# Performance work log

Hardware: AMD Instinct MI355X
Metric: run time of the kernel (lower is better)

The kernel has to match this reference:

```python
import jax, jax.numpy as jnp
import numpy as np

L = 24; CAP = 2 ** 18; F = 2; POS_DIM = 3; NR_ITERS_C2F = 10000
SCALES = np.geomspace(1.0, 1e-4, L).astype(np.float32)
PRIMES = np.array([1, 2654435761, 805459861], dtype=np.uint32)


def _sh4(d):
    # real spherical harmonics up to degree 4 (l=0..3) -> 16 features
    x, y, z = d[:, 0], d[:, 1], d[:, 2]
    xx, yy, zz = x * x, y * y, z * z
    return jnp.stack([
        jnp.full_like(x, 0.28209479177387814),
        -0.48860251190291987 * y, 0.48860251190291987 * z, -0.48860251190291987 * x,
        1.0925484305920792 * x * y, -1.0925484305920792 * y * z,
        0.94617469575755997 * zz - 0.31539156525251999,
        -1.0925484305920792 * x * z, 0.54627421529603959 * (xx - yy),
        -0.59004358992664352 * y * (3.0 * xx - yy),
        2.8906114426405538 * x * y * z,
        -0.45704579946446572 * y * (4.0 * zz - xx - yy),
        0.37317633259011546 * z * (2.0 * zz - 3.0 * xx - 3.0 * yy),
        -0.45704579946446572 * x * (4.0 * zz - xx - yy),
        1.4453057213202769 * z * (xx - yy),
        -0.59004358992664352 * x * (xx - 3.0 * yy),
    ], axis=1)


def _window(iter_nr):
    # map_range_val(iter,0,C,0.3,1.0) then cosine coarse-to-fine window per level
    t = 0.3 + 0.7 * min(max(float(iter_nr) / NR_ITERS_C2F, 0.0), 1.0)
    return 0.5 * (1.0 - jnp.cos(jnp.pi * jnp.clip(t * L - jnp.arange(L, dtype=jnp.float32), 0.0, 1.0)))


def _encode(pos, tables, shifts, window):
    # multi-res hash encoding: per-level gather of 8 cell corners + linear interp
    scales = jnp.asarray(SCALES)
    coords = pos[None, :, :] / scales[:, None, None]          # [L,N,3]
    fl = jnp.floor(coords)
    frac = coords - fl                                        # [L,N,3]
    base = fl.astype(jnp.int32) + shifts[:, None, :].astype(jnp.int32)
    primes = jnp.asarray(PRIMES)
    out = jnp.zeros((L, pos.shape[0], F), dtype=tables.dtype)
    for corner in range(8):  # fixed small loop over cell corners
        offs = jnp.array([(corner >> k) & 1 for k in range(3)], dtype=jnp.int32)
        c = (base + offs).astype(jnp.uint32)
        h = c * primes
        idx = (h[..., 0] ^ h[..., 1] ^ h[..., 2]) & jnp.uint32(CAP - 1)  # [L,N]
        w = jnp.prod(jnp.where(offs == 1, frac, 1.0 - frac), axis=-1)    # [L,N]
        feat = jax.vmap(lambda t, i: t[i])(tables, idx.astype(jnp.int32))  # [L,N,F] gather
        out = out + w[..., None] * feat
    out = out * window[:, None, None]
    feats = jnp.transpose(out, (1, 0, 2)).reshape(pos.shape[0], L * F)
    return jnp.concatenate([feats, pos], axis=1)  # concat_points, scaling=1 -> [N, 51]


def _lin_init(key, fan_in, fan_out):
    kw, kb = jax.random.split(key)
    w = jax.random.normal(kw, (fan_in, fan_out), dtype=jnp.float32) * np.sqrt(2.0 / fan_in)
    b = jnp.zeros((fan_out,), dtype=jnp.float32)
    return w, b


def setup_inputs() -> dict:
    key = jax.random.key(0)
    ks = jax.random.split(key, 12)
    N = 1 << 20
    samples_pos = jax.random.uniform(ks[0], (N, 3), minval=-1.0, maxval=1.0)
    d = jax.random.normal(ks[1], (N, 3), dtype=jnp.float32)
    samples_dirs = d / jnp.linalg.norm(d, axis=-1, keepdims=True)
    tables = jax.random.uniform(ks[2], (L, CAP, F), minval=-1e-4, maxval=1e-4)
    shifts = jax.random.randint(ks[3], (L, 3), 0, 100000, dtype=jnp.int32)
    W1, b1 = _lin_init(ks[4], 51, 64)
    W2, b2 = _lin_init(ks[5], 64, 64)
    W3, b3 = _lin_init(ks[6], 64, 64)
    W4, b4 = _lin_init(ks[7], 64, 65)
    R1, rb1 = _lin_init(ks[8], 80, 64)
    R2, rb2 = _lin_init(ks[9], 64, 64)
    R3, rb3 = _lin_init(ks[10], 64, 3)
    return dict(samples_pos=samples_pos, samples_dirs=samples_dirs, iter_nr=10000,
                tables=tables, shifts=shifts,
                W1=W1, b1=b1, W2=W2, b2=b2, W3=W3, b3=b3, W4=W4, b4=b4,
                R1=R1, rb1=rb1, R2=R2, rb2=rb2, R3=R3, rb3=rb3)


def reference(samples_pos, samples_dirs, iter_nr, tables, shifts,
              W1, b1, W2, b2, W3, b3, W4, b4, R1, rb1, R2, rb2, R3, rb3):
    window = _window(iter_nr)
    pf = _encode(samples_pos, tables, shifts, window)           # [N,51]
    sh = _sh4(samples_dirs)                                     # [N,16] (no grad in original)
    g = lambda x: jax.nn.gelu(x, approximate=False)             # torch GELU default = exact
    h = g(pf @ W1 + b1)
    h = g(h @ W2 + b2)
    h = g(h @ W3 + b3)
    fd = h @ W4 + b4                                            # [N,65]
    density = jax.nn.softplus(fd[:, 0:1])
    feat_rgb = fd[:, 1:65]
    hr = jnp.concatenate([g(feat_rgb), sh], axis=1)             # [N,80]
    hr = g(hr @ R1 + rb1)
    hr = g(hr @ R2 + rb2)
    rgb = jax.nn.sigmoid(hr @ R3 + rb3)                         # [N,3]
    return rgb, density
```

## Files before the change

kernel.cpp:

```cpp
#include <hip/hip_runtime.h>
#include <math.h>

typedef unsigned short u16;
typedef unsigned int   u32;

#define LVLS 24
#define CAPN (1 << 18)
#define STR  84
#define WAVES 8
#define TPW  16
#define ACTSZ (TPW * STR + 16)

#define WB1   0
#define WB2   4096
#define WB3   8192
#define WB4   12288
#define WBR1  16384
#define WBR2  22528
#define SWOFF 26624
#define W4C   26672
#define R3C   26736
#define SHF   26928
#define ACT0  27008
#define LDS_U32 (ACT0 + WAVES * ACTSZ)

typedef float    f32x4 __attribute__((ext_vector_type(4)));
typedef _Float16 f16x8 __attribute__((ext_vector_type(8)));
typedef u32      u32x4 __attribute__((ext_vector_type(4)));

#if __has_builtin(__builtin_amdgcn_rcpf)
#define RCPF(x) __builtin_amdgcn_rcpf(x)
#else
#define RCPF(x) (1.0f / (x))
#endif
#if __has_builtin(__builtin_amdgcn_exp2f)
#define EXP2F(x) __builtin_amdgcn_exp2f(x)
#else
#define EXP2F(x) exp2f(x)
#endif


__device__ __forceinline__ float h2f(u16 b) {
    union { u16 u; _Float16 h; } v; v.u = b; return (float)v.h;
}
__device__ __forceinline__ u16 f2h(float x) {
    union { _Float16 h; u16 u; } v; v.h = (_Float16)x; return v.u;
}
__device__ __forceinline__ void hsplit(float x, u16& h, u16& l) {
    h = f2h(x);
    float r = x - h2f(h);
    l = f2h(r);
}
__device__ __forceinline__ u32 packhl(float x) {
    u16 h, l; hsplit(x, h, l);
    return ((u32)h << 16) | l;
}
__device__ __forceinline__ float unpackhl(u32 w) {
    return h2f((u16)(w >> 16)) + h2f((u16)(w & 0xffffu));
}
__device__ __forceinline__ float gelu_f(float x) {
    float z  = fabsf(x) * 0.70710678118654752f;
    float t  = RCPF(fmaf(0.3275911f, z, 1.0f));
    float e  = EXP2F(-z * z * 1.44269504088896340f);
    float p  = fmaf(1.061405429f, t, -1.453152027f);
    p = fmaf(p, t, 1.421413741f);
    p = fmaf(p, t, -0.284496736f);
    p = fmaf(p, t, 0.254829592f);
    p = p * t;
    float erfv = fmaf(-p, e, 1.0f);
    float se   = copysignf(erfv, x);
    return x * fmaf(0.5f, se, 0.5f);
}
__device__ __forceinline__ float sigmoid_f(float y) {
    return RCPF(1.0f + EXP2F(-y * 1.44269504088896340f));
}
__device__ __forceinline__ f16x8 cast8h(u32 a, u32 b, u32 c, u32 d) {
    union { u32 u[4]; f16x8 h; } v; v.u[0]=a; v.u[1]=b; v.u[2]=c; v.u[3]=d; return v.h;
}
__device__ __forceinline__ f16x8 cast8hv(u32x4 u) {
    union { u32x4 u4; f16x8 h; } v; v.u4 = u; return v.h;
}
__device__ __forceinline__ void window_scale(int l, const int* iter, float& sc, float& wl) {
    sc = powf(10.0f, (float)l * (-4.0f / 23.0f));
    double itd = (double)iter[0] / 10000.0;
    itd = itd < 0.0 ? 0.0 : (itd > 1.0 ? 1.0 : itd);
    float tL = (float)((0.3 + 0.7 * itd) * 24.0);
    float arg = fminf(fmaxf(tL - (float)l, 0.0f), 1.0f);
    wl = 0.5f - 0.5f * cosf(3.14159265358979323846f * arg);
}

__device__ __forceinline__ void hash_level(float px, float py, float pz, float sc, float wl,
                                           int sx, int sy, int sz,
                                           const float* __restrict__ tl,
                                           float& f0, float& f1) {
    float cx = px / sc, cy = py / sc, cz = pz / sc;
    float fx = floorf(cx), fy = floorf(cy), fz = floorf(cz);
    float rx = cx - fx, ry = cy - fy, rz = cz - fz;
    int bx = (int)fx + sx, by = (int)fy + sy, bz = (int)fz + sz;
    u32 hx0 = (u32)bx, hx1 = (u32)(bx + 1);
    u32 hy0 = (u32)by * 2654435761u, hy1 = (u32)(by + 1) * 2654435761u;
    u32 hz0 = (u32)bz * 805459861u,  hz1 = (u32)(bz + 1) * 805459861u;
    float a0 = 0.f, a1 = 0.f;
    #pragma unroll
    for (int c = 0; c < 8; c++) {
        u32 hx = (c & 1) ? hx1 : hx0;
        u32 hy = (c & 2) ? hy1 : hy0;
        u32 hz = (c & 4) ? hz1 : hz0;
        u32 idx = (hx ^ hy ^ hz) & (CAPN - 1);
        float w = ((c & 1) ? rx : 1.0f - rx);
        w *= ((c & 2) ? ry : 1.0f - ry);
        w *= ((c & 4) ? rz : 1.0f - rz);
        float2 tf = *(const float2*)(tl + 2 * (size_t)idx);
        a0 = fmaf(w, tf.x, a0);
        a1 = fmaf(w, tf.y, a1);
    }
    f0 = a0 * wl;
    f1 = a1 * wl;
}

__device__ __forceinline__ void hash_level_part(float px, float py, float pz, float sc,
                                                int sx, int sy, int sz, int c0,
                                                const float* __restrict__ tl,
                                                float2& g0, float2& g1, float& w0, float& w1) {
    float cx = px / sc, cy = py / sc, cz = pz / sc;
    float fx = floorf(cx), fy = floorf(cy), fz = floorf(cz);
    float rx = cx - fx, ry = cy - fy, rz = cz - fz;
    int bx = (int)fx + sx, by = (int)fy + sy, bz = (int)fz + sz;
    #pragma unroll
    for (int cc = 0; cc < 2; cc++) {
        int c = c0 + cc;
        u32 hx = (u32)(bx + (c & 1));
        u32 hy = (u32)(by + ((c >> 1) & 1)) * 2654435761u;
        u32 hz = (u32)(bz + ((c >> 2) & 1)) * 805459861u;
        u32 idx = (hx ^ hy ^ hz) & (CAPN - 1);
        float w = ((c & 1) ? rx : 1.0f - rx)
                * ((c & 2) ? ry : 1.0f - ry)
                * ((c & 4) ? rz : 1.0f - rz);
        float2 tf = *(const float2*)(tl + 2 * (size_t)idx);
        if (cc == 0) { g0 = tf; w0 = w; } else { g1 = tf; w1 = w; }
    }
}

__device__ __forceinline__ void wavesync() {
    asm volatile("s_waitcnt lgkmcnt(0)" ::: "memory");
    __builtin_amdgcn_sched_barrier(0);
}

template <int NKT, bool SHT>
__device__ __forceinline__ void mfma_layer_lds(const u32* blob, const u32* actw,
                                               int lane, f32x4 acc[4]) {
    const int q = lane >> 4, r = lane & 15;
    const int half = NKT * 1024;
    #pragma unroll
    for (int it = 0; it < 4; it++) acc[it] = (f32x4){0.f, 0.f, 0.f, 0.f};
    #pragma unroll
    for (int kt = 0; kt < NKT; kt++) {
        f16x8 whi[4], wlo[4];
        #pragma unroll
        for (int it = 0; it < 4; it++) {
            const u32* pb = blob + ((it * NKT + kt) * 64 + lane) * 4;
            whi[it] = cast8hv(*(const u32x4*)pb);
            wlo[it] = cast8hv(*(const u32x4*)(pb + half));
        }
        bool zero = SHT && (kt == NKT - 1) && (q >= 2);
        const u32* rowp = actw + r * STR + kt * 32 + q * 8;
        u32x4 v0 = *(const u32x4*)rowp;
        u32x4 v1 = *(const u32x4*)(rowp + 4);
        if (zero) { v0 = (u32x4){0,0,0,0}; v1 = (u32x4){0,0,0,0}; }
        u32 v[8] = { v0.x, v0.y, v0.z, v0.w, v1.x, v1.y, v1.z, v1.w };
        u32 xh[4], xl[4];
        #pragma unroll
        for (int j2 = 0; j2 < 4; j2++) {
            xh[j2] = (v[2*j2] >> 16) | (v[2*j2+1] & 0xffff0000u);
            xl[j2] = (v[2*j2] & 0xffffu) | (v[2*j2+1] << 16);
        }
        f16x8 bh = cast8h(xh[0], xh[1], xh[2], xh[3]);
        f16x8 bl = cast8h(xl[0], xl[1], xl[2], xl[3]);
        #pragma unroll
        for (int it = 0; it < 4; it++) {
            acc[it] = __builtin_amdgcn_mfma_f32_16x16x32_f16(whi[it], bh, acc[it], 0, 0, 0);
            acc[it] = __builtin_amdgcn_mfma_f32_16x16x32_f16(whi[it], bl, acc[it], 0, 0, 0);
            acc[it] = __builtin_amdgcn_mfma_f32_16x16x32_f16(wlo[it], bh, acc[it], 0, 0, 0);
        }
    }
}

__device__ __forceinline__ void epilogue_gelu(f32x4 acc[4], const float* __restrict__ bias,
                                              u32* actw, int lane) {
    const int q = lane >> 4, r = lane & 15;
    #pragma unroll
    for (int it = 0; it < 4; it++) {
        int mb = it * 16 + q * 4;
        float c0 = bias[mb], c1 = bias[mb + 1], c2 = bias[mb + 2], c3 = bias[mb + 3];
        f32x4 d = acc[it];
        u32x4 wv;
        wv.x = packhl(gelu_f(fmaf(d[0], 0x1p-16f, c0)) * 256.0f);
        wv.y = packhl(gelu_f(fmaf(d[1], 0x1p-16f, c1)) * 256.0f);
        wv.z = packhl(gelu_f(fmaf(d[2], 0x1p-16f, c2)) * 256.0f);
        wv.w = packhl(gelu_f(fmaf(d[3], 0x1p-16f, c3)) * 256.0f);
        *(u32x4*)(actw + r * STR + mb) = wv;
    }
}

template <bool SPLIT>
__global__ void __launch_bounds__(512, 1) nerf_persist(
    const float* __restrict__ pos, const float* __restrict__ dirs,
    const int* __restrict__ iter, const float* __restrict__ tables,
    const int* __restrict__ shifts,
    const float* __restrict__ W1, const float* __restrict__ b1,
    const float* __restrict__ W2, const float* __restrict__ b2,
    const float* __restrict__ W3, const float* __restrict__ b3,
    const float* __restrict__ W4, const float* __restrict__ b4,
    const float* __restrict__ R1, const float* __restrict__ rb1,
    const float* __restrict__ R2, const float* __restrict__ rb2,
    const float* __restrict__ R3, const float* __restrict__ rb3,
    u32* __restrict__ pf,
    float* __restrict__ out, int n, int nbat, int ppb)
{
    extern __shared__ u32 lds[];
    const int tid  = threadIdx.x;
    const int lane = tid & 63;
    const int wave = tid >> 6;
    const int r = lane & 15;
    const int h = lane >> 4;

    {
        const float* Wp[6] = { W1, W2, W3, W4, R1, R2 };
        for (int e2 = tid; e2 < 13312; e2 += 512) {
            int p = e2, base, nkt, Ksrc, ldm, coloff, layer;
            if      (p < 2048)  { layer=0; base=WB1;  nkt=2; Ksrc=51; ldm=64; coloff=0; }
            else if (p < 4096)  { layer=1; base=WB2;  nkt=2; Ksrc=64; ldm=64; coloff=0; p-=2048; }
            else if (p < 6144)  { layer=2; base=WB3;  nkt=2; Ksrc=64; ldm=64; coloff=0; p-=4096; }
            else if (p < 8192)  { layer=3; base=WB4;  nkt=2; Ksrc=64; ldm=65; coloff=1; p-=6144; }
            else if (p < 11264) { layer=4; base=WBR1; nkt=3; Ksrc=80; ldm=64; coloff=0; p-=8192; }
            else                { layer=5; base=WBR2; nkt=2; Ksrc=64; ldm=64; coloff=0; p-=11264; }
            const float* W = Wp[layer];
            int j = p & 3, ln = (p >> 2) & 63, fk = p >> 8;
            int qq = ln >> 4, rr = ln & 15;
            int kt = fk % nkt, it = fk / nkt;
            int m  = it * 16 + rr;
            int k0 = kt * 32 + qq * 8 + 2 * j;
            float w0 = (k0     < Ksrc) ? W[(size_t)k0 * ldm + m + coloff] * 256.0f : 0.0f;
            float w1 = (k0 + 1 < Ksrc) ? W[(size_t)(k0 + 1) * ldm + m + coloff] * 256.0f : 0.0f;
            u16 h0, l0, h1, l1; hsplit(w0, h0, l0); hsplit(w1, h1, l1);
            int half = nkt * 1024;
            int idx  = base + (fk * 64 + ln) * 4 + j;
            lds[idx]        = (u32)h0 | ((u32)h1 << 16);
            lds[idx + half] = (u32)l0 | ((u32)l1 << 16);
        }
        if (tid < 24) {
            float sc, wl; window_scale(tid, iter, sc, wl);
            lds[SWOFF + 2*tid]     = __float_as_uint(sc);
            lds[SWOFF + 2*tid + 1] = __float_as_uint(wl);
        }
        if (tid >= 64 && tid < 128)  lds[W4C + tid - 64]  = __float_as_uint(W4[(size_t)(tid - 64) * 65]);
        if (tid >= 128 && tid < 320) lds[R3C + tid - 128] = __float_as_uint(R3[tid - 128]);
        if (tid >= 320 && tid < 392) lds[SHF + tid - 320] = (u32)shifts[tid - 320];
    }
    __syncthreads();

    u32* actw  = lds + ACT0 + wave * ACTSZ;
    u32* myrow = actw + r * STR;

    const int pbase = SPLIT ? blockIdx.x * ppb : 0;

    if constexpr (SPLIT) {
        for (int cp = 0; cp < ppb; cp += 512 * 8) {
            float lx[8], ly[8], lz[8];
            bool  lv[8];
            #pragma unroll
            for (int j = 0; j < 8; j++) {
                int off = cp + j * 512 + tid;
                int p = pbase + off;
                lv[j] = (off < ppb) && (p < n);
                lx[j] = 0.f; ly[j] = 0.f; lz[j] = 0.f;
                if (lv[j]) { lx[j] = pos[3*p]; ly[j] = pos[3*p+1]; lz[j] = pos[3*p+2]; }
            }
            for (int l = 0; l < LVLS; l++) {
                float sc = __uint_as_float(lds[SWOFF + 2*l]);
                float wl = __uint_as_float(lds[SWOFF + 2*l + 1]);
                int sx = (int)lds[SHF + 3*l], sy = (int)lds[SHF + 3*l + 1], sz = (int)lds[SHF + 3*l + 2];
                const float* tl = tables + 2 * ((size_t)l * CAPN);
                #pragma unroll 2
                for (int j = 0; j < 8; j++) {
                    if (!lv[j]) continue;
                    float f0, f1;
                    hash_level(lx[j], ly[j], lz[j], sc, wl, sx, sy, sz, tl, f0, f1);
                    int p = pbase + cp + j * 512 + tid;
                    pf[(size_t)l * n + p] = (u32)f2h(f0 * 256.0f) | ((u32)f2h(f1 * 256.0f) << 16);
                }
                __syncthreads();
            }
        }
        __syncthreads();
    }

    const int iters = SPLIT ? (ppb / (WAVES * TPW)) : nbat;
    for (int bb0 = 0; bb0 < iters; bb0++) {
        int tstart;
        if constexpr (SPLIT) {
            tstart = pbase + (bb0 * WAVES + wave) * TPW;
        } else {
            int bb = blockIdx.x + bb0 * gridDim.x;
            if (bb >= nbat) break;
            tstart = (bb * WAVES + wave) * TPW;
        }
        const bool tok = (tstart < n);
        const int i    = tstart + r;
        const bool valid = tok && (i < n);

        float px = 0.f, py = 0.f, pz = 0.f;
        if (valid) { px = pos[3*i]; py = pos[3*i+1]; pz = pos[3*i+2]; }

        if (tok && h == 0) {
            #pragma unroll
            for (int k = 51; k < 64; k++) myrow[k] = 0u;
            myrow[48] = packhl(px * 256.0f);
            myrow[49] = packhl(py * 256.0f);
            myrow[50] = packhl(pz * 256.0f);
        }

        if constexpr (SPLIT) {
            if (tok) {
                #pragma unroll
                for (int li = 0; li < 6; li++) {
                    int l = h * 6 + li;
                    u32 v = valid ? pf[(size_t)l * n + i] : 0u;
                    myrow[2*l]     = v << 16;
                    myrow[2*l + 1] = v & 0xffff0000u;
                }
            }
        } else {
            if (tok) {
                const int c0 = h * 2;
                #pragma unroll 2
                for (int l = 0; l < LVLS; l++) {
                    float sc = __uint_as_float(lds[SWOFF + 2*l]);
                    float wl = __uint_as_float(lds[SWOFF + 2*l + 1]);
                    int sx = (int)lds[SHF + 3*l], sy = (int)lds[SHF + 3*l + 1], sz = (int)lds[SHF + 3*l + 2];
                    float2 g0, g1; float w0, w1;
                    hash_level_part(px, py, pz, sc, sx, sy, sz, c0,
                                    tables + 2 * ((size_t)l * CAPN), g0, g1, w0, w1);
                    float a0 = fmaf(w0, g0.x, w1 * g1.x);
                    float a1 = fmaf(w0, g0.y, w1 * g1.y);
                    a0 += __shfl_xor(a0, 16); a0 += __shfl_xor(a0, 32);
                    a1 += __shfl_xor(a1, 16); a1 += __shfl_xor(a1, 32);
                    if (h == 0) {
                        myrow[2*l]     = (u32)f2h(a0 * wl * 256.0f) << 16;
                        myrow[2*l + 1] = (u32)f2h(a1 * wl * 256.0f) << 16;
                    }
                }
            }
        }
        wavesync();

        f32x4 acc[4];
        if (tok) { mfma_layer_lds<2, false>(lds + WB1, actw, lane, acc); epilogue_gelu(acc, b1, actw, lane); }
        wavesync();
        if (tok) { mfma_layer_lds<2, false>(lds + WB2, actw, lane, acc); epilogue_gelu(acc, b2, actw, lane); }
        wavesync();
        if (tok) { mfma_layer_lds<2, false>(lds + WB3, actw, lane, acc); epilogue_gelu(acc, b3, actw, lane); }
        wavesync();

        if (tok) {
            float t = 0.f;
            #pragma unroll
            for (int kk = 0; kk < 16; kk++) {
                int k = h * 16 + kk;
                t = fmaf(unpackhl(myrow[k]), __uint_as_float(lds[W4C + k]), t);
            }
            t += __shfl_xor(t, 16);
            t += __shfl_xor(t, 32);
            float s = fmaf(t, 0x1p-8f, b4[0]);
            if (h == 0 && valid) out[(size_t)3 * n + i] = fmaxf(s, 0.f) + log1pf(expf(-fabsf(s)));

            mfma_layer_lds<2, false>(lds + WB4, actw, lane, acc);
            epilogue_gelu(acc, b4 + 1, actw, lane);

            float dx = 0.f, dy = 0.f, dz = 0.f;
            if (valid) { dx = dirs[3*i]; dy = dirs[3*i+1]; dz = dirs[3*i+2]; }
            float xx = dx*dx, yy = dy*dy, zz = dz*dz;
            float sh[16];
            sh[0]  = 0.28209479177387814f;
            sh[1]  = -0.48860251190291987f * dy;
            sh[2]  = 0.48860251190291987f * dz;
            sh[3]  = -0.48860251190291987f * dx;
            sh[4]  = 1.0925484305920792f * dx * dy;
            sh[5]  = -1.0925484305920792f * dy * dz;
            sh[6]  = 0.94617469575756f * zz - 0.31539156525252f;
            sh[7]  = -1.0925484305920792f * dx * dz;
            sh[8]  = 0.5462742152960396f * (xx - yy);
            sh[9]  = -0.5900435899266435f * dy * (3.0f * xx - yy);
            sh[10] = 2.890611442640554f * dx * dy * dz;
            sh[11] = -0.4570457994644657f * dy * (4.0f * zz - xx - yy);
            sh[12] = 0.37317633259011546f * dz * (2.0f * zz - 3.0f * xx - 3.0f * yy);
            sh[13] = -0.4570457994644657f * dx * (4.0f * zz - xx - yy);
            sh[14] = 1.445305721320277f * dz * (xx - yy);
            sh[15] = -0.5900435899266435f * dx * (xx - 3.0f * yy);
            #pragma unroll
            for (int j = 0; j < 4; j++) myrow[64 + h * 4 + j] = packhl(sh[h * 4 + j] * 256.0f);
        }
        wavesync();

        if (tok) { mfma_layer_lds<3, true >(lds + WBR1, actw, lane, acc); epilogue_gelu(acc, rb1, actw, lane); }
        wavesync();
        if (tok) { mfma_layer_lds<2, false>(lds + WBR2, actw, lane, acc); epilogue_gelu(acc, rb2, actw, lane); }
        wavesync();

        if (tok) {
            float t0 = 0.f, t1 = 0.f, t2 = 0.f;
            #pragma unroll
            for (int kk = 0; kk < 16; kk++) {
                int k = h * 16 + kk;
                float xv = unpackhl(myrow[k]);
                t0 = fmaf(xv, __uint_as_float(lds[R3C + 3*k + 0]), t0);
                t1 = fmaf(xv, __uint_as_float(lds[R3C + 3*k + 1]), t1);
                t2 = fmaf(xv, __uint_as_float(lds[R3C + 3*k + 2]), t2);
            }
            t0 += __shfl_xor(t0, 16); t0 += __shfl_xor(t0, 32);
            t1 += __shfl_xor(t1, 16); t1 += __shfl_xor(t1, 32);
            t2 += __shfl_xor(t2, 16); t2 += __shfl_xor(t2, 32);
            if (h == 0 && valid) {
                float y0 = fmaf(t0, 0x1p-8f, rb3[0]);
                float y1 = fmaf(t1, 0x1p-8f, rb3[1]);
                float y2 = fmaf(t2, 0x1p-8f, rb3[2]);
                out[(size_t)3 * i + 0] = sigmoid_f(y0);
                out[(size_t)3 * i + 1] = sigmoid_f(y1);
                out[(size_t)3 * i + 2] = sigmoid_f(y2);
            }
        }
        wavesync();
    }
}

extern "C" void kernel_launch(void* const* d_in, const int* in_sizes, int n_in,
                              void* d_out, int out_size, void* d_ws, size_t ws_size,
                              hipStream_t stream) {
    int n = in_sizes[0] / 3;
    int ntiles = (n + TPW - 1) / TPW;
    int nbat = (ntiles + WAVES - 1) / WAVES;
    size_t ldsb = (size_t)LDS_U32 * 4;

    size_t need = (size_t)LVLS * (size_t)n * 4;
    bool split = (ws_size >= need) && (n >= 256 * WAVES * TPW);

    if (split) {
        int cpb = (n + 255) / 256;
        int ppb = (cpb + WAVES * TPW - 1) & ~(WAVES * TPW - 1);
        hipFuncSetAttribute(reinterpret_cast<const void*>(nerf_persist<true>),
                            hipFuncAttributeMaxDynamicSharedMemorySize, (int)ldsb);
        nerf_persist<true><<<256, 512, ldsb, stream>>>(
            (const float*)d_in[0], (const float*)d_in[1], (const int*)d_in[2],
            (const float*)d_in[3], (const int*)d_in[4],
            (const float*)d_in[5],  (const float*)d_in[6],
            (const float*)d_in[7],  (const float*)d_in[8],
            (const float*)d_in[9],  (const float*)d_in[10],
            (const float*)d_in[11], (const float*)d_in[12],
            (const float*)d_in[13], (const float*)d_in[14],
            (const float*)d_in[15], (const float*)d_in[16],
            (const float*)d_in[17], (const float*)d_in[18],
            (u32*)d_ws, (float*)d_out, n, nbat, ppb);
    } else {
        int grid = nbat < 256 ? nbat : 256;
        hipFuncSetAttribute(reinterpret_cast<const void*>(nerf_persist<false>),
                            hipFuncAttributeMaxDynamicSharedMemorySize, (int)ldsb);
        nerf_persist<false><<<grid, 512, ldsb, stream>>>(
            (const float*)d_in[0], (const float*)d_in[1], (const int*)d_in[2],
            (const float*)d_in[3], (const int*)d_in[4],
            (const float*)d_in[5],  (const float*)d_in[6],
            (const float*)d_in[7],  (const float*)d_in[8],
            (const float*)d_in[9],  (const float*)d_in[10],
            (const float*)d_in[11], (const float*)d_in[12],
            (const float*)d_in[13], (const float*)d_in[14],
            (const float*)d_in[15], (const float*)d_in[16],
            (const float*)d_in[17], (const float*)d_in[18],
            (u32*)d_ws, (float*)d_out, n, nbat, 0);
    }
}
```

Before: 1.044 ms.

## Keep MLP activations in registers and exchange via shuffles instead of LDS

Removes the per-wave LDS activation staging between MLP layers. Each layer's epilogue output now stays in registers, and the MFMA B operands are rebuilt with cross-lane shuffles, which also drops the wave-level LDS waits. LDS shrinks to the weights only, so the block grows to 16 waves (1024 threads) and the non-split hash path is restructured so each lane handles whole levels. The cost is more shuffle instructions and much higher register pressure per thread under the 1024-thread launch bound.

```diff
diff --git a/kernel.cpp b/kernel.cpp
--- a/kernel.cpp
+++ b/kernel.cpp
@@ -6,10 +6,8 @@
 
 #define LVLS 24
 #define CAPN (1 << 18)
-#define STR  84
-#define WAVES 8
+#define WAVES 16
 #define TPW  16
-#define ACTSZ (TPW * STR + 16)
 
 #define WB1   0
 #define WB2   4096
@@ -21,8 +19,7 @@
 #define W4C   26672
 #define R3C   26736
 #define SHF   26928
-#define ACT0  27008
-#define LDS_U32 (ACT0 + WAVES * ACTSZ)
+#define LDS_U32 27008
 
 typedef float    f32x4 __attribute__((ext_vector_type(4)));
 typedef _Float16 f16x8 __attribute__((ext_vector_type(8)));
@@ -118,39 +115,14 @@
     f1 = a1 * wl;
 }
 
-__device__ __forceinline__ void hash_level_part(float px, float py, float pz, float sc,
-                                                int sx, int sy, int sz, int c0,
-                                                const float* __restrict__ tl,
-                                                float2& g0, float2& g1, float& w0, float& w1) {
-    float cx = px / sc, cy = py / sc, cz = pz / sc;
-    float fx = floorf(cx), fy = floorf(cy), fz = floorf(cz);
-    float rx = cx - fx, ry = cy - fy, rz = cz - fz;
-    int bx = (int)fx + sx, by = (int)fy + sy, bz = (int)fz + sz;
-    #pragma unroll
-    for (int cc = 0; cc < 2; cc++) {
-        int c = c0 + cc;
-        u32 hx = (u32)(bx + (c & 1));
-        u32 hy = (u32)(by + ((c >> 1) & 1)) * 2654435761u;
-        u32 hz = (u32)(bz + ((c >> 2) & 1)) * 805459861u;
-        u32 idx = (hx ^ hy ^ hz) & (CAPN - 1);
-        float w = ((c & 1) ? rx : 1.0f - rx)
-                * ((c & 2) ? ry : 1.0f - ry)
-                * ((c & 4) ? rz : 1.0f - rz);
-        float2 tf = *(const float2*)(tl + 2 * (size_t)idx);
-        if (cc == 0) { g0 = tf; w0 = w; } else { g1 = tf; w1 = w; }
-    }
-}
-
-__device__ __forceinline__ void wavesync() {
-    asm volatile("s_waitcnt lgkmcnt(0)" ::: "memory");
-    __builtin_amdgcn_sched_barrier(0);
-}
-
-template <int NKT, bool SHT>
-__device__ __forceinline__ void mfma_layer_lds(const u32* blob, const u32* actw,
+template <int NKT>
+__device__ __forceinline__ void mfma_layer_reg(const u32* blob, const u32 E[6][4],
                                                int lane, f32x4 acc[4]) {
     const int q = lane >> 4, r = lane & 15;
     const int half = NKT * 1024;
+    const int src0 = ((q & 1) << 5) + r;
+    const int src1 = src0 + 16;
+    const bool hiq = (q >= 2);
     #pragma unroll
     for (int it = 0; it < 4; it++) acc[it] = (f32x4){0.f, 0.f, 0.f, 0.f};
     #pragma unroll
@@ -162,12 +134,16 @@
             whi[it] = cast8hv(*(const u32x4*)pb);
             wlo[it] = cast8hv(*(const u32x4*)(pb + half));
         }
-        bool zero = SHT && (kt == NKT - 1) && (q >= 2);
-        const u32* rowp = actw + r * STR + kt * 32 + q * 8;
-        u32x4 v0 = *(const u32x4*)rowp;
-        u32x4 v1 = *(const u32x4*)(rowp + 4);
-        if (zero) { v0 = (u32x4){0,0,0,0}; v1 = (u32x4){0,0,0,0}; }
-        u32 v[8] = { v0.x, v0.y, v0.z, v0.w, v1.x, v1.y, v1.z, v1.w };
+        u32 v[8];
+        #pragma unroll
+        for (int j = 0; j < 4; j++) {
+            u32 a0 = (u32)__shfl((int)E[2*kt][j],     src0);
+            u32 a1 = (u32)__shfl((int)E[2*kt + 1][j], src0);
+            u32 b0 = (u32)__shfl((int)E[2*kt][j],     src1);
+            u32 b1 = (u32)__shfl((int)E[2*kt + 1][j], src1);
+            v[j]     = hiq ? a1 : a0;
+            v[j + 4] = hiq ? b1 : b0;
+        }
         u32 xh[4], xl[4];
         #pragma unroll
         for (int j2 = 0; j2 < 4; j2++) {
@@ -185,25 +161,23 @@
     }
 }
 
-__device__ __forceinline__ void epilogue_gelu(f32x4 acc[4], const float* __restrict__ bias,
-                                              u32* actw, int lane) {
-    const int q = lane >> 4, r = lane & 15;
+__device__ __forceinline__ void epilogue_reg(f32x4 acc[4], const float* __restrict__ bias,
+                                             int lane, u32 E[6][4]) {
+    const int q = lane >> 4;
     #pragma unroll
     for (int it = 0; it < 4; it++) {
         int mb = it * 16 + q * 4;
         float c0 = bias[mb], c1 = bias[mb + 1], c2 = bias[mb + 2], c3 = bias[mb + 3];
         f32x4 d = acc[it];
-        u32x4 wv;
-        wv.x = packhl(gelu_f(fmaf(d[0], 0x1p-16f, c0)) * 256.0f);
-        wv.y = packhl(gelu_f(fmaf(d[1], 0x1p-16f, c1)) * 256.0f);
-        wv.z = packhl(gelu_f(fmaf(d[2], 0x1p-16f, c2)) * 256.0f);
-        wv.w = packhl(gelu_f(fmaf(d[3], 0x1p-16f, c3)) * 256.0f);
-        *(u32x4*)(actw + r * STR + mb) = wv;
+        E[it][0] = packhl(gelu_f(fmaf(d[0], 0x1p-16f, c0)) * 256.0f);
+        E[it][1] = packhl(gelu_f(fmaf(d[1], 0x1p-16f, c1)) * 256.0f);
+        E[it][2] = packhl(gelu_f(fmaf(d[2], 0x1p-16f, c2)) * 256.0f);
+        E[it][3] = packhl(gelu_f(fmaf(d[3], 0x1p-16f, c3)) * 256.0f);
     }
 }
 
 template <bool SPLIT>
-__global__ void __launch_bounds__(512, 1) nerf_persist(
+__global__ void __launch_bounds__(1024) nerf_persist(
     const float* __restrict__ pos, const float* __restrict__ dirs,
     const int* __restrict__ iter, const float* __restrict__ tables,
     const int* __restrict__ shifts,
@@ -222,11 +196,11 @@
     const int lane = tid & 63;
     const int wave = tid >> 6;
     const int r = lane & 15;
-    const int h = lane >> 4;
+    const int q = lane >> 4;
 
     {
         const float* Wp[6] = { W1, W2, W3, W4, R1, R2 };
-        for (int e2 = tid; e2 < 13312; e2 += 512) {
+        for (int e2 = tid; e2 < 13312; e2 += 1024) {
             int p = e2, base, nkt, Ksrc, ldm, coloff, layer;
             if      (p < 2048)  { layer=0; base=WB1;  nkt=2; Ksrc=51; ldm=64; coloff=0; }
             else if (p < 4096)  { layer=1; base=WB2;  nkt=2; Ksrc=64; ldm=64; coloff=0; p-=2048; }
@@ -259,18 +233,15 @@
     }
     __syncthreads();
 
-    u32* actw  = lds + ACT0 + wave * ACTSZ;
-    u32* myrow = actw + r * STR;
-
     const int pbase = SPLIT ? blockIdx.x * ppb : 0;
 
     if constexpr (SPLIT) {
-        for (int cp = 0; cp < ppb; cp += 512 * 8) {
-            float lx[8], ly[8], lz[8];
-            bool  lv[8];
-            #pragma unroll
-            for (int j = 0; j < 8; j++) {
-                int off = cp + j * 512 + tid;
+        for (int cp = 0; cp < ppb; cp += 1024 * 4) {
+            float lx[4], ly[4], lz[4];
+            bool  lv[4];
+            #pragma unroll
+            for (int j = 0; j < 4; j++) {
+                int off = cp + j * 1024 + tid;
                 int p = pbase + off;
                 lv[j] = (off < ppb) && (p < n);
                 lx[j] = 0.f; ly[j] = 0.f; lz[j] = 0.f;
@@ -282,11 +253,11 @@
                 int sx = (int)lds[SHF + 3*l], sy = (int)lds[SHF + 3*l + 1], sz = (int)lds[SHF + 3*l + 2];
                 const float* tl = tables + 2 * ((size_t)l * CAPN);
                 #pragma unroll 2
-                for (int j = 0; j < 8; j++) {
+                for (int j = 0; j < 4; j++) {
                     if (!lv[j]) continue;
                     float f0, f1;
                     hash_level(lx[j], ly[j], lz[j], sc, wl, sx, sy, sz, tl, f0, f1);
-                    int p = pbase + cp + j * 512 + tid;
+                    int p = pbase + cp + j * 1024 + tid;
                     pf[(size_t)l * n + p] = (u32)f2h(f0 * 256.0f) | ((u32)f2h(f1 * 256.0f) << 16);
                 }
                 __syncthreads();
@@ -305,78 +276,78 @@
             if (bb >= nbat) break;
             tstart = (bb * WAVES + wave) * TPW;
         }
-        const bool tok = (tstart < n);
+        if (tstart >= n) continue;
         const int i    = tstart + r;
-        const bool valid = tok && (i < n);
+        const bool valid = (i < n);
 
         float px = 0.f, py = 0.f, pz = 0.f;
         if (valid) { px = pos[3*i]; py = pos[3*i+1]; pz = pos[3*i+2]; }
 
-        if (tok && h == 0) {
-            #pragma unroll
-            for (int k = 51; k < 64; k++) myrow[k] = 0u;
-            myrow[48] = packhl(px * 256.0f);
-            myrow[49] = packhl(py * 256.0f);
-            myrow[50] = packhl(pz * 256.0f);
-        }
+        u32 E[6][4];
+        #pragma unroll
+        for (int j = 0; j < 4; j++) { E[4][j] = 0u; E[5][j] = 0u; }
 
         if constexpr (SPLIT) {
-            if (tok) {
+            #pragma unroll
+            for (int it = 0; it < 3; it++) {
+                int l0 = it * 8 + q * 2;
+                u32 v0 = valid ? pf[(size_t)l0 * n + i] : 0u;
+                u32 v1 = valid ? pf[(size_t)(l0 + 1) * n + i] : 0u;
+                E[it][0] = v0 << 16;
+                E[it][1] = v0 & 0xffff0000u;
+                E[it][2] = v1 << 16;
+                E[it][3] = v1 & 0xffff0000u;
+            }
+        } else {
+            #pragma unroll
+            for (int it = 0; it < 3; it++) {
                 #pragma unroll
-                for (int li = 0; li < 6; li++) {
-                    int l = h * 6 + li;
-                    u32 v = valid ? pf[(size_t)l * n + i] : 0u;
-                    myrow[2*l]     = v << 16;
-                    myrow[2*l + 1] = v & 0xffff0000u;
+                for (int dl = 0; dl < 2; dl++) {
+                    int l = it * 8 + q * 2 + dl;
+                    float sc = __uint_as_float(lds[SWOFF + 2*l]);
+                    float wl = __uint_as_float(lds[SWOFF + 2*l + 1]);
+                    float f0, f1;
+                    hash_level(px, py, pz, sc, wl,
+                               (int)lds[SHF + 3*l], (int)lds[SHF + 3*l + 1], (int)lds[SHF + 3*l + 2],
+                               tables + 2 * ((size_t)l * CAPN), f0, f1);
+                    E[it][2*dl]     = (u32)f2h(f0 * 256.0f) << 16;
+                    E[it][2*dl + 1] = (u32)f2h(f1 * 256.0f) << 16;
                 }
             }
+        }
+        if (q == 0) {
+            E[3][0] = packhl(px * 256.0f);
+            E[3][1] = packhl(py * 256.0f);
+            E[3][2] = packhl(pz * 256.0f);
+            E[3][3] = 0u;
         } else {
-            if (tok) {
-                const int c0 = h * 2;
-                #pragma unroll 2
-                for (int l = 0; l < LVLS; l++) {
-                    float sc = __uint_as_float(lds[SWOFF + 2*l]);
-                    float wl = __uint_as_float(lds[SWOFF + 2*l + 1]);
-                    int sx = (int)lds[SHF + 3*l], sy = (int)lds[SHF + 3*l + 1], sz = (int)lds[SHF + 3*l + 2];
-                    float2 g0, g1; float w0, w1;
-                    hash_level_part(px, py, pz, sc, sx, sy, sz, c0,
-                                    tables + 2 * ((size_t)l * CAPN), g0, g1, w0, w1);
-                    float a0 = fmaf(w0, g0.x, w1 * g1.x);
-                    float a1 = fmaf(w0, g0.y, w1 * g1.y);
-                    a0 += __shfl_xor(a0, 16); a0 += __shfl_xor(a0, 32);
-                    a1 += __shfl_xor(a1, 16); a1 += __shfl_xor(a1, 32);
-                    if (h == 0) {
-                        myrow[2*l]     = (u32)f2h(a0 * wl * 256.0f) << 16;
-                        myrow[2*l + 1] = (u32)f2h(a1 * wl * 256.0f) << 16;
-                    }
-                }
-            }
-        }
-        wavesync();
+            #pragma unroll
+            for (int j = 0; j < 4; j++) E[3][j] = 0u;
+        }
 
         f32x4 acc[4];
-        if (tok) { mfma_layer_lds<2, false>(lds + WB1, actw, lane, acc); epilogue_gelu(acc, b1, actw, lane); }
-        wavesync();
-        if (tok) { mfma_layer_lds<2, false>(lds + WB2, actw, lane, acc); epilogue_gelu(acc, b2, actw, lane); }
-        wavesync();
-        if (tok) { mfma_layer_lds<2, false>(lds + WB3, actw, lane, acc); epilogue_gelu(acc, b3, actw, lane); }
-        wavesync();
-
-        if (tok) {
+        mfma_layer_reg<2>(lds + WB1, E, lane, acc); epilogue_reg(acc, b1, lane, E);
+        mfma_layer_reg<2>(lds + WB2, E, lane, acc); epilogue_reg(acc, b2, lane, E);
+        mfma_layer_reg<2>(lds + WB3, E, lane, acc); epilogue_reg(acc, b3, lane, E);
+
+        {
             float t = 0.f;
             #pragma unroll
-            for (int kk = 0; kk < 16; kk++) {
-                int k = h * 16 + kk;
-                t = fmaf(unpackhl(myrow[k]), __uint_as_float(lds[W4C + k]), t);
-            }
+            for (int it = 0; it < 4; it++)
+                #pragma unroll
+                for (int j = 0; j < 4; j++)
+                    t = fmaf(unpackhl(E[it][j]),
+                             __uint_as_float(lds[W4C + it * 16 + q * 4 + j]), t);
             t += __shfl_xor(t, 16);
             t += __shfl_xor(t, 32);
             float s = fmaf(t, 0x1p-8f, b4[0]);
-            if (h == 0 && valid) out[(size_t)3 * n + i] = fmaxf(s, 0.f) + log1pf(expf(-fabsf(s)));
-
-            mfma_layer_lds<2, false>(lds + WB4, actw, lane, acc);
-            epilogue_gelu(acc, b4 + 1, actw, lane);
-
+            if (q == 0 && valid) out[(size_t)3 * n + i] = fmaxf(s, 0.f) + log1pf(expf(-fabsf(s)));
+        }
+
+        mfma_layer_reg<2>(lds + WB4, E, lane, acc);
+        epilogue_reg(acc, b4 + 1, lane, E);
+
+        {
             float dx = 0.f, dy = 0.f, dz = 0.f;
             if (valid) { dx = dirs[3*i]; dy = dirs[3*i+1]; dz = dirs[3*i+2]; }
             float xx = dx*dx, yy = dy*dy, zz = dz*dz;
@@ -398,29 +369,30 @@
             sh[14] = 1.445305721320277f * dz * (xx - yy);
             sh[15] = -0.5900435899266435f * dx * (xx - 3.0f * yy);
             #pragma unroll
-            for (int j = 0; j < 4; j++) myrow[64 + h * 4 + j] = packhl(sh[h * 4 + j] * 256.0f);
-        }
-        wavesync();
-
-        if (tok) { mfma_layer_lds<3, true >(lds + WBR1, actw, lane, acc); epilogue_gelu(acc, rb1, actw, lane); }
-        wavesync();
-        if (tok) { mfma_layer_lds<2, false>(lds + WBR2, actw, lane, acc); epilogue_gelu(acc, rb2, actw, lane); }
-        wavesync();
-
-        if (tok) {
+            for (int j = 0; j < 4; j++) E[4][j] = packhl(sh[q * 4 + j] * 256.0f);
+        }
+
+        mfma_layer_reg<3>(lds + WBR1, E, lane, acc);
+        epilogue_reg(acc, rb1, lane, E);
+        mfma_layer_reg<2>(lds + WBR2, E, lane, acc);
+        epilogue_reg(acc, rb2, lane, E);
+
+        {
             float t0 = 0.f, t1 = 0.f, t2 = 0.f;
             #pragma unroll
-            for (int kk = 0; kk < 16; kk++) {
-                int k = h * 16 + kk;
-                float xv = unpackhl(myrow[k]);
-                t0 = fmaf(xv, __uint_as_float(lds[R3C + 3*k + 0]), t0);
-                t1 = fmaf(xv, __uint_as_float(lds[R3C + 3*k + 1]), t1);
-                t2 = fmaf(xv, __uint_as_float(lds[R3C + 3*k + 2]), t2);
-            }
+            for (int it = 0; it < 4; it++)
+                #pragma unroll
+                for (int j = 0; j < 4; j++) {
+                    int f = it * 16 + q * 4 + j;
+                    float xv = unpackhl(E[it][j]);
+                    t0 = fmaf(xv, __uint_as_float(lds[R3C + 3*f + 0]), t0);
+                    t1 = fmaf(xv, __uint_as_float(lds[R3C + 3*f + 1]), t1);
+                    t2 = fmaf(xv, __uint_as_float(lds[R3C + 3*f + 2]), t2);
+                }
             t0 += __shfl_xor(t0, 16); t0 += __shfl_xor(t0, 32);
             t1 += __shfl_xor(t1, 16); t1 += __shfl_xor(t1, 32);
             t2 += __shfl_xor(t2, 16); t2 += __shfl_xor(t2, 32);
-            if (h == 0 && valid) {
+            if (q == 0 && valid) {
                 float y0 = fmaf(t0, 0x1p-8f, rb3[0]);
                 float y1 = fmaf(t1, 0x1p-8f, rb3[1]);
                 float y2 = fmaf(t2, 0x1p-8f, rb3[2]);
@@ -429,7 +401,6 @@
                 out[(size_t)3 * i + 2] = sigmoid_f(y2);
             }
         }
-        wavesync();
     }
 }
 
@@ -446,10 +417,11 @@
 
     if (split) {
         int cpb = (n + 255) / 256;
-        int ppb = (cpb + WAVES * TPW - 1) & ~(WAVES * TPW - 1);
+        int wtp = WAVES * TPW;
+        int ppb = (cpb + wtp - 1) / wtp * wtp;
         hipFuncSetAttribute(reinterpret_cast<const void*>(nerf_persist<true>),
                             hipFuncAttributeMaxDynamicSharedMemorySize, (int)ldsb);
-        nerf_persist<true><<<256, 512, ldsb, stream>>>(
+        nerf_persist<true><<<256, 1024, ldsb, stream>>>(
             (const float*)d_in[0], (const float*)d_in[1], (const int*)d_in[2],
             (const float*)d_in[3], (const int*)d_in[4],
             (const float*)d_in[5],  (const float*)d_in[6],
@@ -464,7 +436,7 @@
         int grid = nbat < 256 ? nbat : 256;
         hipFuncSetAttribute(reinterpret_cast<const void*>(nerf_persist<false>),
                             hipFuncAttributeMaxDynamicSharedMemorySize, (int)ldsb);
-        nerf_persist<false><<<grid, 512, ldsb, stream>>>(
+        nerf_persist<false><<<grid, 1024, ldsb, stream>>>(
             (const float*)d_in[0], (const float*)d_in[1], (const int*)d_in[2],
             (const float*)d_in[3], (const int*)d_in[4],
             (const float*)d_in[5],  (const float*)d_in[6],
```

New measurement: 1.022 ms. 1.02x faster.
